# Performance work log

Measured on AMD Instinct MI355X. Metric: run time of the kernel, lower is better.

The kernel has to match this reference:

```python
import jax, jax.numpy as jnp
import numpy as np

NUM_USERS = 50000
NUM_ITEMS = 20000
NUM_NODES = NUM_USERS + NUM_ITEMS
FEAT_DIM = 768
HID = 128
NUM_LAYERS = 3
N_EDGES = 2_000_000
LN_EPS = 1e-5


def setup_inputs() -> dict:
    key = jax.random.key(0)
    ks = jax.random.split(key, 12)
    edge_index = jax.random.randint(ks[0], (2, N_EDGES), 0, NUM_NODES, dtype=jnp.int64) if jax.config.jax_enable_x64 else jax.random.randint(ks[0], (2, N_EDGES), 0, NUM_NODES, dtype=jnp.int32)
    item_features = jax.random.normal(ks[1], (NUM_ITEMS, FEAT_DIM), dtype=jnp.float32)
    embedding = jax.random.normal(ks[2], (NUM_NODES, HID), dtype=jnp.float32) * 0.1
    W1 = jax.random.normal(ks[3], (FEAT_DIM, 512), dtype=jnp.float32) * 0.02
    b1 = jnp.zeros((512,), jnp.float32)
    g1 = jnp.ones((512,), jnp.float32)
    be1 = jnp.zeros((512,), jnp.float32)
    W2 = jax.random.normal(ks[4], (512, HID), dtype=jnp.float32) * 0.02
    b2 = jnp.zeros((HID,), jnp.float32)
    g2 = jnp.ones((HID,), jnp.float32)
    be2 = jnp.zeros((HID,), jnp.float32)
    W3 = jax.random.normal(ks[5], (HID, HID), dtype=jnp.float32) * 0.02
    b3 = jnp.zeros((HID,), jnp.float32)
    meta_weight = jnp.asarray(0.01, jnp.float32)
    return {"edge_index": edge_index, "item_features": item_features, "embedding": embedding,
            "W1": W1, "b1": b1, "g1": g1, "be1": be1,
            "W2": W2, "b2": b2, "g2": g2, "be2": be2,
            "W3": W3, "b3": b3, "meta_weight": meta_weight}


def _layer_norm(x, g, b):
    mu = jnp.mean(x, axis=-1, keepdims=True)
    var = jnp.mean(jnp.square(x - mu), axis=-1, keepdims=True)
    return (x - mu) * jax.lax.rsqrt(var + LN_EPS) * g + b


def reference(edge_index, item_features, embedding, W1, b1, g1, be1, W2, b2, g2, be2, W3, b3, meta_weight):
    # item metadata MLP (eval mode: dropout is identity)
    h = jax.nn.relu(_layer_norm(item_features @ W1 + b1, g1, be1))
    h = jax.nn.relu(_layer_norm(h @ W2 + b2, g2, be2))
    h = h @ W3 + b3
    # F.normalize(p=2, dim=-1)
    item_meta = h / jnp.maximum(jnp.linalg.norm(h, axis=-1, keepdims=True), 1e-12)

    # fuse metadata into item id embeddings
    e0 = jnp.concatenate([embedding[:NUM_USERS],
                          embedding[NUM_USERS:] + meta_weight * item_meta], axis=0)

    src, dst = edge_index[0], edge_index[1]
    # symmetric GCN normalization: deg from destination counts
    deg = jax.ops.segment_sum(jnp.ones(src.shape[0], e0.dtype), dst, num_segments=NUM_NODES)
    dinv = jnp.where(deg > 0, jax.lax.rsqrt(jnp.maximum(deg, 1.0)), 0.0)
    norm = (dinv[src] * dinv[dst])[:, None]  # [E, 1]

    alpha = 1.0 / (NUM_LAYERS + 1)
    out = e0 * alpha
    x = e0
    for _ in range(NUM_LAYERS):
        x = jax.ops.segment_sum(x[src] * norm, dst, num_segments=NUM_NODES)
        out = out + x * alpha
    return out
```

## Files before the change

### kernel.cpp

```cpp
#include <hip/hip_runtime.h>
#include <hip/hip_bf16.h>

#define NUM_USERS 50000
#define NUM_ITEMS 20000
#define NUM_NODES (NUM_USERS + NUM_ITEMS)
#define FEAT_DIM 768
#define HID 128
#define H1DIM 512
#define LN_EPS 1e-5f
#define ALPHA 0.25f
#define NBKT 137

typedef __attribute__((ext_vector_type(8))) short short8;
typedef __attribute__((ext_vector_type(4))) float floatx4;

static __device__ inline unsigned short f2bf(float f) {
  unsigned int u = __float_as_uint(f);
  u += 0x7fffu + ((u >> 16) & 1u);
  return (unsigned short)(u >> 16);
}
static __device__ inline float bflo(unsigned int u) {
  return __uint_as_float(u << 16);
}
static __device__ inline float bfhi(unsigned int u) {
  return __uint_as_float(u & 0xffff0000u);
}

__global__ __launch_bounds__(256) void cast_bf16(
    const float* __restrict__ in, unsigned short* __restrict__ out) {
  size_t i = (size_t)blockIdx.x * 256 + threadIdx.x;
  float4 u = ((const float4*)in)[i * 2];
  float4 v = ((const float4*)in)[i * 2 + 1];
  union { unsigned short s[8]; uint4 q; } p;
  p.s[0] = f2bf(u.x); p.s[1] = f2bf(u.y); p.s[2] = f2bf(u.z); p.s[3] = f2bf(u.w);
  p.s[4] = f2bf(v.x); p.s[5] = f2bf(v.y); p.s[6] = f2bf(v.z); p.s[7] = f2bf(v.w);
  ((uint4*)out)[i] = p.q;
}

__global__ __launch_bounds__(256) void transpose_cast(
    const float* __restrict__ W, unsigned short* __restrict__ Wt,
    int K, int N) {
  __shared__ float tile[32][33];
  int tx = threadIdx.x, ty = threadIdx.y;
  int bx = blockIdx.x, by = blockIdx.y;
#pragma unroll
  for (int kk = 0; kk < 4; kk++)
    tile[ty + kk * 8][tx] = W[(size_t)(by * 32 + ty + kk * 8) * N + bx * 32 + tx];
  __syncthreads();
#pragma unroll
  for (int kk = 0; kk < 4; kk++)
    Wt[(size_t)(bx * 32 + ty + kk * 8) * K + by * 32 + tx] =
        f2bf(tile[tx][ty + kk * 8]);
}

__global__ __launch_bounds__(256) void gemm_mfma_bias(
    const unsigned short* __restrict__ A, const unsigned short* __restrict__ Bt,
    const float* __restrict__ bias, float* __restrict__ C,
    int M, int N, int K) {
  __shared__ __align__(16) unsigned short As[128 * 32];
  __shared__ __align__(16) unsigned short Bs[128 * 32];
  const int tid = threadIdx.x;
  const int wave = tid >> 6, lane = tid & 63;
  const int quad = lane >> 4, l16 = lane & 15;
  const int wm = wave >> 1, wn = wave & 1;
  const int bm = blockIdx.y * 128, bn = blockIdx.x * 128;

  floatx4 acc[4][4];
#pragma unroll
  for (int i = 0; i < 4; i++)
#pragma unroll
    for (int j = 0; j < 4; j++) acc[i][j] = (floatx4){0.f, 0.f, 0.f, 0.f};

  const int srow = lane >> 2;
  const int scol = (lane & 3) * 8;

  for (int k0 = 0; k0 < K; k0 += 32) {
#pragma unroll
    for (int i = 0; i < 2; i++) {
      int c = wave * 2 + i;
      int arow = bm + c * 16 + srow;
      if (arow >= M) arow = M - 1;
      const unsigned short* ga = A + (size_t)arow * K + k0 + scol;
      __builtin_amdgcn_global_load_lds(
          (const __attribute__((address_space(1))) unsigned int*)(uintptr_t)ga,
          (__attribute__((address_space(3))) unsigned int*)(uintptr_t)(As + c * 512),
          16, 0, 0);
      int brow = bn + c * 16 + srow;
      const unsigned short* gb = Bt + (size_t)brow * K + k0 + scol;
      __builtin_amdgcn_global_load_lds(
          (const __attribute__((address_space(1))) unsigned int*)(uintptr_t)gb,
          (__attribute__((address_space(3))) unsigned int*)(uintptr_t)(Bs + c * 512),
          16, 0, 0);
    }
    __syncthreads();

    short8 af[4], bf[4];
#pragma unroll
    for (int i = 0; i < 4; i++) {
      af[i] = *(const short8*)&As[(wm * 64 + i * 16 + l16) * 32 + quad * 8];
      bf[i] = *(const short8*)&Bs[(wn * 64 + i * 16 + l16) * 32 + quad * 8];
    }
#pragma unroll
    for (int i = 0; i < 4; i++)
#pragma unroll
      for (int j = 0; j < 4; j++)
        acc[i][j] = __builtin_amdgcn_mfma_f32_16x16x32_bf16(af[i], bf[j],
                                                            acc[i][j], 0, 0, 0);
    __syncthreads();
  }

#pragma unroll
  for (int i = 0; i < 4; i++) {
    int row0 = bm + wm * 64 + i * 16 + quad * 4;
#pragma unroll
    for (int j = 0; j < 4; j++) {
      int col = bn + wn * 64 + j * 16 + l16;
      float bv = bias[col];
#pragma unroll
      for (int r = 0; r < 4; r++) {
        int row = row0 + r;
        if (row < M) C[(size_t)row * N + col] = acc[i][j][r] + bv;
      }
    }
  }
}

__global__ __launch_bounds__(256) void ln_relu_w512_bf16(
    const float* __restrict__ X, const float* __restrict__ g,
    const float* __restrict__ be, unsigned short* __restrict__ O) {
  int row = blockIdx.x, t = threadIdx.x;
  const float* x = X + (size_t)row * H1DIM;
  float v0 = x[t], v1 = x[t + 256];
  float s = v0 + v1, q = v0 * v0 + v1 * v1;
#pragma unroll
  for (int off = 32; off > 0; off >>= 1) {
    s += __shfl_down(s, off);
    q += __shfl_down(q, off);
  }
  __shared__ float ss[4], qq[4];
  int lane = t & 63, wid = t >> 6;
  if (lane == 0) { ss[wid] = s; qq[wid] = q; }
  __syncthreads();
  float S = ss[0] + ss[1] + ss[2] + ss[3];
  float Q = qq[0] + qq[1] + qq[2] + qq[3];
  float mu = S * (1.f / 512.f);
  float var = Q * (1.f / 512.f) - mu * mu;
  float rs = rsqrtf(var + LN_EPS);
  float y0 = (v0 - mu) * rs * g[t] + be[t];
  float y1 = (v1 - mu) * rs * g[t + 256] + be[t + 256];
  unsigned short* o = O + (size_t)row * H1DIM;
  o[t] = f2bf(fmaxf(y0, 0.f));
  o[t + 256] = f2bf(fmaxf(y1, 0.f));
}

__global__ __launch_bounds__(256) void ln_relu_w128(
    float* __restrict__ X, const float* __restrict__ g,
    const float* __restrict__ be, int rows) {
  int gwid = (blockIdx.x * blockDim.x + threadIdx.x) >> 6;
  if (gwid >= rows) return;
  int lane = threadIdx.x & 63;
  float* x = X + (size_t)gwid * HID;
  float v0 = x[lane], v1 = x[lane + 64];
  float s = v0 + v1, q = v0 * v0 + v1 * v1;
#pragma unroll
  for (int off = 32; off > 0; off >>= 1) {
    s += __shfl_down(s, off);
    q += __shfl_down(q, off);
  }
  s = __shfl(s, 0);
  q = __shfl(q, 0);
  float mu = s * (1.f / 128.f);
  float var = q * (1.f / 128.f) - mu * mu;
  float rs = rsqrtf(var + LN_EPS);
  float y0 = (v0 - mu) * rs * g[lane] + be[lane];
  float y1 = (v1 - mu) * rs * g[lane + 64] + be[lane + 64];
  x[lane] = fmaxf(y0, 0.f);
  x[lane + 64] = fmaxf(y1, 0.f);
}

__global__ __launch_bounds__(128) void gemm3_norm4(
    const float* __restrict__ H, const float* __restrict__ W3,
    const float* __restrict__ b3, float* __restrict__ meta) {
  int r0 = blockIdx.x * 4, t = threadIdx.x;
  __shared__ float hrow[4][HID];
#pragma unroll
  for (int r = 0; r < 4; r++) hrow[r][t] = H[(size_t)(r0 + r) * HID + t];
  __syncthreads();
  float s0 = 0.f, s1 = 0.f, s2 = 0.f, s3 = 0.f;
#pragma unroll 4
  for (int k = 0; k < HID; k++) {
    float w = W3[k * HID + t];
    s0 = fmaf(hrow[0][k], w, s0);
    s1 = fmaf(hrow[1][k], w, s1);
    s2 = fmaf(hrow[2][k], w, s2);
    s3 = fmaf(hrow[3][k], w, s3);
  }
  float b = b3[t];
  s0 += b; s1 += b; s2 += b; s3 += b;
  float q0 = s0 * s0, q1 = s1 * s1, q2 = s2 * s2, q3 = s3 * s3;
#pragma unroll
  for (int off = 32; off > 0; off >>= 1) {
    q0 += __shfl_down(q0, off);
    q1 += __shfl_down(q1, off);
    q2 += __shfl_down(q2, off);
    q3 += __shfl_down(q3, off);
  }
  __shared__ float qs[4][2];
  if ((t & 63) == 0) {
    int w = t >> 6;
    qs[0][w] = q0; qs[1][w] = q1; qs[2][w] = q2; qs[3][w] = q3;
  }
  __syncthreads();
  float n0 = fmaxf(sqrtf(qs[0][0] + qs[0][1]), 1e-12f);
  float n1 = fmaxf(sqrtf(qs[1][0] + qs[1][1]), 1e-12f);
  float n2 = fmaxf(sqrtf(qs[2][0] + qs[2][1]), 1e-12f);
  float n3 = fmaxf(sqrtf(qs[3][0] + qs[3][1]), 1e-12f);
  meta[(size_t)(r0 + 0) * HID + t] = s0 / n0;
  meta[(size_t)(r0 + 1) * HID + t] = s1 / n1;
  meta[(size_t)(r0 + 2) * HID + t] = s2 / n2;
  meta[(size_t)(r0 + 3) * HID + t] = s3 / n3;
}

__global__ __launch_bounds__(256) void build_e0_cm4(
    const float* __restrict__ emb, const float* __restrict__ meta,
    const float* __restrict__ mw_p, unsigned int* __restrict__ x0c,
    float* __restrict__ out) {
  size_t i = (size_t)blockIdx.x * 256 + threadIdx.x;
  int node = (int)(i >> 6);
  int u6 = (int)(i & 63);
  int chunk = u6 >> 4, fl = u6 & 15;
  int f0 = chunk * 32 + fl * 2;
  float2 e = *(const float2*)&emb[(size_t)node * HID + f0];
  if (node >= NUM_USERS) {
    float2 m = *(const float2*)&meta[(size_t)(node - NUM_USERS) * HID + f0];
    float w = mw_p[0];
    e.x += w * m.x;
    e.y += w * m.y;
  }
  *(float2*)&out[(size_t)node * HID + f0] = make_float2(ALPHA * e.x, ALPHA * e.y);
  unsigned pk = (unsigned)f2bf(e.x) | ((unsigned)f2bf(e.y) << 16);
  x0c[((size_t)chunk * NUM_NODES + node) * 16 + fl] = pk;
}

__global__ __launch_bounds__(256) void p1_hist(const int* __restrict__ dst,
                                               int* __restrict__ ghist,
                                               int E, int NBL) {
  __shared__ int h[NBKT];
  int t = threadIdx.x;
  if (t < NBKT) h[t] = 0;
  __syncthreads();
  int base = blockIdx.x * 8192;
  for (int i = t; i < 8192; i += 256) {
    int e = base + i;
    if (e < E) atomicAdd(&h[dst[e] >> 9], 1);
  }
  __syncthreads();
  if (t < NBKT) ghist[t * NBL + blockIdx.x] = h[t];
}

__global__ __launch_bounds__(256) void scan_a(const int* __restrict__ in,
                                              int* __restrict__ outp,
                                              int* __restrict__ bsum, int n) {
  int i = blockIdx.x * 256 + threadIdx.x;
  int v = (i < n) ? in[i] : 0;
  int lane = threadIdx.x & 63, wid = threadIdx.x >> 6;
  int s = v;
#pragma unroll
  for (int off = 1; off < 64; off <<= 1) {
    int u = __shfl_up(s, off);
    if (lane >= off) s += u;
  }
  __shared__ int wsum[4];
  if (lane == 63) wsum[wid] = s;
  __syncthreads();
  int add = 0;
  for (int w = 0; w < wid; w++) add += wsum[w];
  int incl = s + add;
  if (i < n) outp[i] = incl - v;
  if (threadIdx.x == 255) bsum[blockIdx.x] = incl;
}

__global__ __launch_bounds__(512) void scan_b(int* __restrict__ bsum, int nb) {
  int t = threadIdx.x;
  int v = (t < nb) ? bsum[t] : 0;
  int lane = t & 63, wid = t >> 6;
  int s = v;
#pragma unroll
  for (int off = 1; off < 64; off <<= 1) {
    int u = __shfl_up(s, off);
    if (lane >= off) s += u;
  }
  __shared__ int ws[8];
  if (lane == 63) ws[wid] = s;
  __syncthreads();
  int add = 0;
  for (int w = 0; w < wid; w++) add += ws[w];
  if (t < nb) bsum[t] = s + add - v;
}

__global__ __launch_bounds__(256) void scan_c(int* __restrict__ outp,
                                              const int* __restrict__ bsum,
                                              int n) {
  int i = blockIdx.x * 256 + threadIdx.x;
  if (i < n) outp[i] += bsum[blockIdx.x];
}

__global__ __launch_bounds__(256) void p1_scatter(
    const int* __restrict__ src, const int* __restrict__ dst,
    const int* __restrict__ gscan, unsigned long long* __restrict__ pairs,
    int E, int NBL) {
  __shared__ int cur[NBKT];
  int t = threadIdx.x;
  if (t < NBKT) cur[t] = gscan[t * NBL + blockIdx.x];
  __syncthreads();
  int base = blockIdx.x * 8192;
  for (int i = t; i < 8192; i += 256) {
    int e = base + i;
    if (e < E) {
      int d = dst[e];
      int pos = atomicAdd(&cur[d >> 9], 1);
      pairs[pos] = ((unsigned long long)(unsigned)d << 32) | (unsigned)src[e];
    }
  }
}

__global__ __launch_bounds__(512) void p2_build(
    const unsigned long long* __restrict__ pairs,
    const int* __restrict__ gscan, int* __restrict__ rowptr,
    int* __restrict__ csr_src, int E, int NBL) {
  __shared__ int hist[512];
  __shared__ int ws8[8];
  int b = blockIdx.x, t = threadIdx.x;
  int base = gscan[b * NBL];
  int end = (b == NBKT - 1) ? E : gscan[(b + 1) * NBL];
  hist[t] = 0;
  __syncthreads();
  for (int i = base + t; i < end; i += 512) {
    unsigned d = (unsigned)(pairs[i] >> 32);
    atomicAdd(&hist[d & 511], 1);
  }
  __syncthreads();
  int v = hist[t];
  int lane = t & 63, wid = t >> 6;
  int s = v;
#pragma unroll
  for (int off = 1; off < 64; off <<= 1) {
    int u = __shfl_up(s, off);
    if (lane >= off) s += u;
  }
  if (lane == 63) ws8[wid] = s;
  __syncthreads();
  int add = 0;
  for (int w = 0; w < wid; w++) add += ws8[w];
  int excl = s + add - v;
  int node = (b << 9) + t;
  if (node < NUM_NODES) rowptr[node] = base + excl;
  if (b == NBKT - 1 && t == 0) rowptr[NUM_NODES] = E;
  __syncthreads();
  hist[t] = base + excl;
  __syncthreads();
  for (int i = base + t; i < end; i += 512) {
    unsigned long long p = pairs[i];
    unsigned d = (unsigned)(p >> 32);
    int pos = atomicAdd(&hist[d & 511], 1);
    csr_src[pos] = (int)(unsigned)p;
  }
}

__global__ __launch_bounds__(256) void calc_dinv2(const int* __restrict__ rowptr,
                                                  float* __restrict__ dinv,
                                                  int n) {
  int i = blockIdx.x * 256 + threadIdx.x;
  if (i < n) {
    int d = rowptr[i + 1] - rowptr[i];
    dinv[i] = d > 0 ? rsqrtf((float)d) : 0.f;
  }
}

__global__ __launch_bounds__(256) void pack_edges(
    const int* __restrict__ csr_src, const float* __restrict__ dinv,
    uint2* __restrict__ epack, int E) {
  int i = blockIdx.x * 256 + threadIdx.x;
  if (i < E) {
    int s = csr_src[i];
    epack[i] = make_uint2((unsigned)s, __float_as_uint(dinv[s]));
  }
}

__global__ __launch_bounds__(256) void spmm_chunk4(
    const int* __restrict__ rowptr, const uint2* __restrict__ epack,
    const float* __restrict__ dinv, const uint2* __restrict__ xc,
    uint2* __restrict__ yc, float* __restrict__ out, int write_y) {
  int chunk = blockIdx.x & 3;
  int rowblk = blockIdx.x >> 2;
  int tid = threadIdx.x;
  int wave = tid >> 6, lane = tid & 63;
  int slot = lane >> 3, fl = lane & 7;
  int row = rowblk * 32 + wave * 8 + slot;
  bool act = row < NUM_NODES;
  int rr = act ? row : NUM_NODES - 1;
  int beg = rowptr[rr], end = rowptr[rr + 1];
  float wd = dinv[rr];
  const uint2* xq = xc + (size_t)chunk * NUM_NODES * 8 + fl;
  float a0 = 0.f, a1 = 0.f, a2 = 0.f, a3 = 0.f;
  int p = beg;
  for (; p + 4 <= end; p += 4) {
    uint2 e0 = epack[p], e1 = epack[p + 1];
    uint2 e2 = epack[p + 2], e3 = epack[p + 3];
    float c0 = __uint_as_float(e0.y), c1 = __uint_as_float(e1.y);
    float c2 = __uint_as_float(e2.y), c3 = __uint_as_float(e3.y);
    uint2 v0 = xq[(size_t)e0.x * 8];
    uint2 v1 = xq[(size_t)e1.x * 8];
    uint2 v2 = xq[(size_t)e2.x * 8];
    uint2 v3 = xq[(size_t)e3.x * 8];
    a0 += c0 * bflo(v0.x) + c1 * bflo(v1.x) + c2 * bflo(v2.x) + c3 * bflo(v3.x);
    a1 += c0 * bfhi(v0.x) + c1 * bfhi(v1.x) + c2 * bfhi(v2.x) + c3 * bfhi(v3.x);
    a2 += c0 * bflo(v0.y) + c1 * bflo(v1.y) + c2 * bflo(v2.y) + c3 * bflo(v3.y);
    a3 += c0 * bfhi(v0.y) + c1 * bfhi(v1.y) + c2 * bfhi(v2.y) + c3 * bfhi(v3.y);
  }
  for (; p < end; p++) {
    uint2 e0 = epack[p];
    float c0 = __uint_as_float(e0.y);
    uint2 v0 = xq[(size_t)e0.x * 8];
    a0 += c0 * bflo(v0.x);
    a1 += c0 * bfhi(v0.x);
    a2 += c0 * bflo(v0.y);
    a3 += c0 * bfhi(v0.y);
  }
  a0 *= wd; a1 *= wd; a2 *= wd; a3 *= wd;
  if (act) {
    if (write_y) {
      unsigned p0 = (unsigned)f2bf(a0) | ((unsigned)f2bf(a1) << 16);
      unsigned p1 = (unsigned)f2bf(a2) | ((unsigned)f2bf(a3) << 16);
      yc[((size_t)chunk * NUM_NODES + row) * 8 + fl] = make_uint2(p0, p1);
    }
    float4* op = (float4*)&out[(size_t)row * HID + chunk * 32 + fl * 4];
    float4 po = *op;
    po.x += ALPHA * a0;
    po.y += ALPHA * a1;
    po.z += ALPHA * a2;
    po.w += ALPHA * a3;
    *op = po;
  }
}

extern "C" void kernel_launch(void* const* d_in, const int* in_sizes, int n_in,
                              void* d_out, int out_size, void* d_ws,
                              size_t ws_size, hipStream_t stream) {
  const int* edge = (const int*)d_in[0];
  const float* item_feat = (const float*)d_in[1];
  const float* emb = (const float*)d_in[2];
  const float* W1 = (const float*)d_in[3];
  const float* b1 = (const float*)d_in[4];
  const float* g1 = (const float*)d_in[5];
  const float* be1 = (const float*)d_in[6];
  const float* W2 = (const float*)d_in[7];
  const float* b2 = (const float*)d_in[8];
  const float* g2 = (const float*)d_in[9];
  const float* be2 = (const float*)d_in[10];
  const float* W3 = (const float*)d_in[11];
  const float* b3 = (const float*)d_in[12];
  const float* mw = (const float*)d_in[13];
  float* out = (float*)d_out;

  const int E = in_sizes[0] / 2;
  const int* src = edge;
  const int* dst = edge + E;
  const int NBL = (E + 8191) / 8192;
  const int nScan = NBKT * NBL;
  const int NBs = (nScan + 255) / 256;

  char* ws = (char*)d_ws;
  float* h1 = (float*)(ws + 0);
  float* h2 = (float*)(ws + 40960000);
  unsigned short* h1b = (unsigned short*)(ws + 51200000);
  uint2* xA = (uint2*)(ws + 51200000);
  unsigned short* Af = (unsigned short*)(ws + 87040000);
  uint2* xB = (uint2*)(ws + 87040000);
  uint2* xC = (uint2*)(ws + 104960000);
  unsigned short* W1t = (unsigned short*)(ws + 122880000);
  unsigned short* W2t = (unsigned short*)(ws + 123666432);
  float* meta = h1;

  unsigned long long* pairs = (unsigned long long*)(ws + 0);
  uint2* epack = (uint2*)(ws + 0);
  int* rowptr = (int*)(ws + 16000000);
  float* dinv = (float*)(ws + 16500000);
  int* ghist = (int*)(ws + 16800000);
  int* gscan = (int*)(ws + 17000000);
  int* bsum = (int*)(ws + 17200000);
  int* csr_src = (int*)(ws + 17500000);

  cast_bf16<<<(NUM_ITEMS * FEAT_DIM / 8) / 256, 256, 0, stream>>>(item_feat, Af);
  transpose_cast<<<dim3(H1DIM / 32, FEAT_DIM / 32), dim3(32, 8), 0, stream>>>(
      W1, W1t, FEAT_DIM, H1DIM);
  transpose_cast<<<dim3(HID / 32, H1DIM / 32), dim3(32, 8), 0, stream>>>(
      W2, W2t, H1DIM, HID);

  gemm_mfma_bias<<<dim3(H1DIM / 128, (NUM_ITEMS + 127) / 128), 256, 0, stream>>>(
      Af, W1t, b1, h1, NUM_ITEMS, H1DIM, FEAT_DIM);
  ln_relu_w512_bf16<<<NUM_ITEMS, 256, 0, stream>>>(h1, g1, be1, h1b);
  gemm_mfma_bias<<<dim3(HID / 128, (NUM_ITEMS + 127) / 128), 256, 0, stream>>>(
      h1b, W2t, b2, h2, NUM_ITEMS, HID, H1DIM);
  ln_relu_w128<<<(NUM_ITEMS * 64) / 256, 256, 0, stream>>>(h2, g2, be2,
                                                           NUM_ITEMS);
  gemm3_norm4<<<NUM_ITEMS / 4, 128, 0, stream>>>(h2, W3, b3, meta);

  build_e0_cm4<<<(NUM_NODES * 64) / 256, 256, 0, stream>>>(
      emb, meta, mw, (unsigned int*)xA, out);

  p1_hist<<<NBL, 256, 0, stream>>>(dst, ghist, E, NBL);
  scan_a<<<NBs, 256, 0, stream>>>(ghist, gscan, bsum, nScan);
  scan_b<<<1, 512, 0, stream>>>(bsum, NBs);
  scan_c<<<NBs, 256, 0, stream>>>(gscan, bsum, nScan);
  p1_scatter<<<NBL, 256, 0, stream>>>(src, dst, gscan, pairs, E, NBL);
  p2_build<<<NBKT, 512, 0, stream>>>(pairs, gscan, rowptr, csr_src, E, NBL);
  calc_dinv2<<<(NUM_NODES + 255) / 256, 256, 0, stream>>>(rowptr, dinv,
                                                          NUM_NODES);
  pack_edges<<<(E + 255) / 256, 256, 0, stream>>>(csr_src, dinv, epack, E);

  const int RG = ((NUM_NODES + 31) / 32) * 4;
  spmm_chunk4<<<RG, 256, 0, stream>>>(rowptr, epack, dinv, xA, xB, out, 1);
  spmm_chunk4<<<RG, 256, 0, stream>>>(rowptr, epack, dinv, xB, xC, out, 1);
  spmm_chunk4<<<RG, 256, 0, stream>>>(rowptr, epack, dinv, xC, nullptr, out, 0);
}
```

Measured before the change: 619.9 us.

## Fold source-degree scaling into stored features and drop per-edge weights

The input features are pre-scaled by dinv[src], and each layer's output is stored as dinv^2 * acc, so SpMM no longer needs a per-edge coefficient. This removes the pack_edges kernel and halves edge-stream traffic by reading plain int indices with vectorized 8-wide nontemporal loads. The out read-modify-write also uses nontemporal accesses. Because the stored bf16 values now carry an extra dinv factor, rounding error may shift slightly. The build_e0 kernel moves after the degree computation, and meta moves to a separate workspace offset so it does not alias the pairs buffer.

```diff
diff --git a/kernel.cpp b/kernel.cpp
--- a/kernel.cpp
+++ b/kernel.cpp
@@ -13,6 +13,7 @@
 
 typedef __attribute__((ext_vector_type(8))) short short8;
 typedef __attribute__((ext_vector_type(4))) float floatx4;
+typedef __attribute__((ext_vector_type(4))) unsigned int uintx4;
 
 static __device__ inline unsigned short f2bf(float f) {
   unsigned int u = __float_as_uint(f);
@@ -223,8 +224,8 @@
 
 __global__ __launch_bounds__(256) void build_e0_cm4(
     const float* __restrict__ emb, const float* __restrict__ meta,
-    const float* __restrict__ mw_p, unsigned int* __restrict__ x0c,
-    float* __restrict__ out) {
+    const float* __restrict__ mw_p, const float* __restrict__ dinv,
+    unsigned int* __restrict__ x0c, float* __restrict__ out) {
   size_t i = (size_t)blockIdx.x * 256 + threadIdx.x;
   int node = (int)(i >> 6);
   int u6 = (int)(i & 63);
@@ -238,7 +239,8 @@
     e.y += w * m.y;
   }
   *(float2*)&out[(size_t)node * HID + f0] = make_float2(ALPHA * e.x, ALPHA * e.y);
-  unsigned pk = (unsigned)f2bf(e.x) | ((unsigned)f2bf(e.y) << 16);
+  float d = dinv[node];
+  unsigned pk = (unsigned)f2bf(d * e.x) | ((unsigned)f2bf(d * e.y) << 16);
   x0c[((size_t)chunk * NUM_NODES + node) * 16 + fl] = pk;
 }
 
@@ -377,18 +379,16 @@
   }
 }
 
-__global__ __launch_bounds__(256) void pack_edges(
-    const int* __restrict__ csr_src, const float* __restrict__ dinv,
-    uint2* __restrict__ epack, int E) {
-  int i = blockIdx.x * 256 + threadIdx.x;
-  if (i < E) {
-    int s = csr_src[i];
-    epack[i] = make_uint2((unsigned)s, __float_as_uint(dinv[s]));
-  }
-}
+#define ACC1(v)                 \
+  {                             \
+    a0 += bflo((v).x);          \
+    a1 += bfhi((v).x);          \
+    a2 += bflo((v).y);          \
+    a3 += bfhi((v).y);          \
+  }
 
 __global__ __launch_bounds__(256) void spmm_chunk4(
-    const int* __restrict__ rowptr, const uint2* __restrict__ epack,
+    const int* __restrict__ rowptr, const int* __restrict__ csrc,
     const float* __restrict__ dinv, const uint2* __restrict__ xc,
     uint2* __restrict__ yc, float* __restrict__ out, int write_y) {
   int chunk = blockIdx.x & 3;
@@ -404,43 +404,55 @@
   const uint2* xq = xc + (size_t)chunk * NUM_NODES * 8 + fl;
   float a0 = 0.f, a1 = 0.f, a2 = 0.f, a3 = 0.f;
   int p = beg;
-  for (; p + 4 <= end; p += 4) {
-    uint2 e0 = epack[p], e1 = epack[p + 1];
-    uint2 e2 = epack[p + 2], e3 = epack[p + 3];
-    float c0 = __uint_as_float(e0.y), c1 = __uint_as_float(e1.y);
-    float c2 = __uint_as_float(e2.y), c3 = __uint_as_float(e3.y);
-    uint2 v0 = xq[(size_t)e0.x * 8];
-    uint2 v1 = xq[(size_t)e1.x * 8];
-    uint2 v2 = xq[(size_t)e2.x * 8];
-    uint2 v3 = xq[(size_t)e3.x * 8];
-    a0 += c0 * bflo(v0.x) + c1 * bflo(v1.x) + c2 * bflo(v2.x) + c3 * bflo(v3.x);
-    a1 += c0 * bfhi(v0.x) + c1 * bfhi(v1.x) + c2 * bfhi(v2.x) + c3 * bfhi(v3.x);
-    a2 += c0 * bflo(v0.y) + c1 * bflo(v1.y) + c2 * bflo(v2.y) + c3 * bflo(v3.y);
-    a3 += c0 * bfhi(v0.y) + c1 * bfhi(v1.y) + c2 * bfhi(v2.y) + c3 * bfhi(v3.y);
+  int na = (beg + 3) & ~3;
+  if (na > end) na = end;
+  for (; p < na; p++) {
+    int s = __builtin_nontemporal_load(csrc + p);
+    uint2 v = xq[(size_t)(unsigned)s * 8];
+    ACC1(v)
+  }
+  for (; p + 8 <= end; p += 8) {
+    uintx4 sA = __builtin_nontemporal_load((const uintx4*)(csrc + p));
+    uintx4 sB = __builtin_nontemporal_load((const uintx4*)(csrc + p + 4));
+    uint2 v0 = xq[(size_t)sA.x * 8];
+    uint2 v1 = xq[(size_t)sA.y * 8];
+    uint2 v2 = xq[(size_t)sA.z * 8];
+    uint2 v3 = xq[(size_t)sA.w * 8];
+    uint2 v4 = xq[(size_t)sB.x * 8];
+    uint2 v5 = xq[(size_t)sB.y * 8];
+    uint2 v6 = xq[(size_t)sB.z * 8];
+    uint2 v7 = xq[(size_t)sB.w * 8];
+    ACC1(v0) ACC1(v1) ACC1(v2) ACC1(v3)
+    ACC1(v4) ACC1(v5) ACC1(v6) ACC1(v7)
+  }
+  if (p + 4 <= end) {
+    uintx4 sA = __builtin_nontemporal_load((const uintx4*)(csrc + p));
+    uint2 v0 = xq[(size_t)sA.x * 8];
+    uint2 v1 = xq[(size_t)sA.y * 8];
+    uint2 v2 = xq[(size_t)sA.z * 8];
+    uint2 v3 = xq[(size_t)sA.w * 8];
+    ACC1(v0) ACC1(v1) ACC1(v2) ACC1(v3)
+    p += 4;
   }
   for (; p < end; p++) {
-    uint2 e0 = epack[p];
-    float c0 = __uint_as_float(e0.y);
-    uint2 v0 = xq[(size_t)e0.x * 8];
-    a0 += c0 * bflo(v0.x);
-    a1 += c0 * bfhi(v0.x);
-    a2 += c0 * bflo(v0.y);
-    a3 += c0 * bfhi(v0.y);
-  }
-  a0 *= wd; a1 *= wd; a2 *= wd; a3 *= wd;
+    int s = __builtin_nontemporal_load(csrc + p);
+    uint2 v = xq[(size_t)(unsigned)s * 8];
+    ACC1(v)
+  }
+  float y0 = wd * a0, y1 = wd * a1, y2 = wd * a2, y3 = wd * a3;
   if (act) {
     if (write_y) {
-      unsigned p0 = (unsigned)f2bf(a0) | ((unsigned)f2bf(a1) << 16);
-      unsigned p1 = (unsigned)f2bf(a2) | ((unsigned)f2bf(a3) << 16);
+      unsigned p0 = (unsigned)f2bf(wd * y0) | ((unsigned)f2bf(wd * y1) << 16);
+      unsigned p1 = (unsigned)f2bf(wd * y2) | ((unsigned)f2bf(wd * y3) << 16);
       yc[((size_t)chunk * NUM_NODES + row) * 8 + fl] = make_uint2(p0, p1);
     }
-    float4* op = (float4*)&out[(size_t)row * HID + chunk * 32 + fl * 4];
-    float4 po = *op;
-    po.x += ALPHA * a0;
-    po.y += ALPHA * a1;
-    po.z += ALPHA * a2;
-    po.w += ALPHA * a3;
-    *op = po;
+    float* op = &out[(size_t)row * HID + chunk * 32 + fl * 4];
+    floatx4 po = __builtin_nontemporal_load((const floatx4*)op);
+    po.x += ALPHA * y0;
+    po.y += ALPHA * y1;
+    po.z += ALPHA * y2;
+    po.w += ALPHA * y3;
+    __builtin_nontemporal_store(po, (floatx4*)op);
   }
 }
 
@@ -480,10 +492,9 @@
   uint2* xC = (uint2*)(ws + 104960000);
   unsigned short* W1t = (unsigned short*)(ws + 122880000);
   unsigned short* W2t = (unsigned short*)(ws + 123666432);
-  float* meta = h1;
+  float* meta = (float*)(ws + 26000000);
 
   unsigned long long* pairs = (unsigned long long*)(ws + 0);
-  uint2* epack = (uint2*)(ws + 0);
   int* rowptr = (int*)(ws + 16000000);
   float* dinv = (float*)(ws + 16500000);
   int* ghist = (int*)(ws + 16800000);
@@ -506,9 +517,6 @@
                                                            NUM_ITEMS);
   gemm3_norm4<<<NUM_ITEMS / 4, 128, 0, stream>>>(h2, W3, b3, meta);
 
-  build_e0_cm4<<<(NUM_NODES * 64) / 256, 256, 0, stream>>>(
-      emb, meta, mw, (unsigned int*)xA, out);
-
   p1_hist<<<NBL, 256, 0, stream>>>(dst, ghist, E, NBL);
   scan_a<<<NBs, 256, 0, stream>>>(ghist, gscan, bsum, nScan);
   scan_b<<<1, 512, 0, stream>>>(bsum, NBs);
@@ -517,10 +525,12 @@
   p2_build<<<NBKT, 512, 0, stream>>>(pairs, gscan, rowptr, csr_src, E, NBL);
   calc_dinv2<<<(NUM_NODES + 255) / 256, 256, 0, stream>>>(rowptr, dinv,
                                                           NUM_NODES);
-  pack_edges<<<(E + 255) / 256, 256, 0, stream>>>(csr_src, dinv, epack, E);
+
+  build_e0_cm4<<<(NUM_NODES * 64) / 256, 256, 0, stream>>>(
+      emb, meta, mw, dinv, (unsigned int*)xA, out);
 
   const int RG = ((NUM_NODES + 31) / 32) * 4;
-  spmm_chunk4<<<RG, 256, 0, stream>>>(rowptr, epack, dinv, xA, xB, out, 1);
-  spmm_chunk4<<<RG, 256, 0, stream>>>(rowptr, epack, dinv, xB, xC, out, 1);
-  spmm_chunk4<<<RG, 256, 0, stream>>>(rowptr, epack, dinv, xC, nullptr, out, 0);
-}
+  spmm_chunk4<<<RG, 256, 0, stream>>>(rowptr, csr_src, dinv, xA, xB, out, 1);
+  spmm_chunk4<<<RG, 256, 0, stream>>>(rowptr, csr_src, dinv, xB, xC, out, 1);
+  spmm_chunk4<<<RG, 256, 0, stream>>>(rowptr, csr_src, dinv, xC, nullptr, out, 0);
+}
```

Result: slower. 697.5 us (+12.5%).
